# Optimization experiments

Measured on AMD Instinct MI355X. Metric: run time of the kernel, lower is better.

Reference implementation:

```python
import jax, jax.numpy as jnp
import numpy as np

NUM_HEADS = 4
EPS = 1e-5

def _proj(x, W, b):
    # 1x1x1 Conv3d == channel-wise linear: x [B,C,H,W,D], W [Cout,Cin], b [Cout]
    return jnp.einsum('oc,bchwd->bohwd', W, x) + b[None, :, None, None, None]

def setup_inputs() -> dict:
    key = jax.random.key(0)
    ks = jax.random.split(key, 12)
    B, C, H, W, D = 2, 128, 16, 16, 16
    s = 1.0 / np.sqrt(C)
    inp = {
        'query_features': jax.random.normal(ks[0], (B, C, H, W, D), jnp.float32),
        'key_value_features': jax.random.normal(ks[1], (B, C, H, W, D), jnp.float32),
        'Wq': jax.random.normal(ks[2], (C, C), jnp.float32) * s,
        'bq': jax.random.normal(ks[3], (C,), jnp.float32) * 0.01,
        'Wk': jax.random.normal(ks[4], (C, C), jnp.float32) * s,
        'bk': jax.random.normal(ks[5], (C,), jnp.float32) * 0.01,
        'Wv': jax.random.normal(ks[6], (C, C), jnp.float32) * s,
        'bv': jax.random.normal(ks[7], (C,), jnp.float32) * 0.01,
        'Wo': jax.random.normal(ks[8], (C, C), jnp.float32) * s,
        'bo': jax.random.normal(ks[9], (C,), jnp.float32) * 0.01,
    }
    return inp

def reference(query_features, key_value_features, Wq, bq, Wk, bk, Wv, bv, Wo, bo):
    B, C, H, W, D = query_features.shape
    hd = C // NUM_HEADS  # head_dim
    N = H * W * D
    Q = _proj(query_features, Wq, bq).reshape(B, NUM_HEADS, hd, N)
    K = _proj(key_value_features, Wk, bk).reshape(B, NUM_HEADS, hd, N)
    V = _proj(key_value_features, Wv, bv).reshape(B, NUM_HEADS, hd, N)
    scale = hd ** -0.5
    attn = jnp.einsum('bhdn,bhdm->bhnm', Q, K) * scale  # [B,h,N,N]
    attn = jax.nn.softmax(attn, axis=-1)
    out = jnp.einsum('bhnm,bhdm->bhdn', attn, V).reshape(B, C, H, W, D)
    out = _proj(out, Wo, bo)
    res = query_features + out
    # InstanceNorm3d (affine=False): normalize over spatial dims per (B,C)
    mu = jnp.mean(res, axis=(2, 3, 4), keepdims=True)
    var = jnp.var(res, axis=(2, 3, 4), keepdims=True)
    return (res - mu) * jax.lax.rsqrt(var + EPS)
```

## Files before the change

### kernel.cpp

```cpp
#include <hip/hip_runtime.h>
#include <hip/hip_bf16.h>

typedef unsigned short u16;
typedef unsigned int u32;
typedef __bf16 bf16_t;
typedef bf16_t bf16x8 __attribute__((ext_vector_type(8)));
typedef float f32x4 __attribute__((ext_vector_type(4)));

#define NTOT 4096
#define CCH 128
#define QSCL 0.25503486703f

__device__ __forceinline__ float bf2f(u16 x) {
    return __uint_as_float(((u32)x) << 16);
}
__device__ __forceinline__ u32 pkbf(float a, float b) {
    __hip_bfloat162 h = __float22bfloat162_rn(make_float2(a, b));
    u32 r; __builtin_memcpy(&r, &h, 4); return r;
}
__device__ __forceinline__ u16 f2bf(float a) {
    return (u16)(pkbf(a, a) & 0xffffu);
}

__global__ __launch_bounds__(256, 4) void proj_kernel(
    const float* __restrict__ xq, const float* __restrict__ xkv,
    const float* __restrict__ Wq, const float* __restrict__ bq_,
    const float* __restrict__ Wk, const float* __restrict__ bk_,
    const float* __restrict__ Wv, const float* __restrict__ bv_,
    u16* __restrict__ Qt, u16* __restrict__ Kt, u16* __restrict__ Vn)
{
    const int nt = blockIdx.x, p = blockIdx.y, b = blockIdx.z;
    const float* X    = (p == 0) ? xq : xkv;
    const float* W    = (p == 0) ? Wq : (p == 1) ? Wk : Wv;
    const float* bias = (p == 0) ? bq_ : (p == 1) ? bk_ : bv_;
    const float scl   = (p == 0) ? QSCL : 1.0f;
    const int n0 = nt * 64;
    const int tid = threadIdx.x;

    __shared__ u16 Xt[64 * 128];
    __shared__ u16 Wl[128 * 136];

    #pragma unroll
    for (int k = 0; k < 4; ++k) {
        int n = tid & 63;
        int c = (tid >> 6) + k * 4;
        float f[8];
        #pragma unroll
        for (int j = 0; j < 8; ++j)
            f[j] = X[((size_t)(b * CCH) + 8 * c + j) * NTOT + n0 + n];
        uint4 vv = {pkbf(f[0], f[1]), pkbf(f[2], f[3]), pkbf(f[4], f[5]), pkbf(f[6], f[7])};
        *(uint4*)(Xt + n * 128 + ((c ^ (n & 7)) * 8)) = vv;
    }
    #pragma unroll
    for (int k = 0; k < 8; ++k) {
        int id = tid + k * 256;
        int row = id >> 4;
        int off = (id & 15) * 8;
        const float* wsrc = W + (size_t)row * 128 + off;
        float4 f0 = *(const float4*)(wsrc);
        float4 f1 = *(const float4*)(wsrc + 4);
        uint4 vv = {pkbf(f0.x * scl, f0.y * scl), pkbf(f0.z * scl, f0.w * scl),
                    pkbf(f1.x * scl, f1.y * scl), pkbf(f1.z * scl, f1.w * scl)};
        *(uint4*)(Wl + row * 136 + off) = vv;
    }
    __syncthreads();

    const int wave = tid >> 6, lane = tid & 63;
    const int quad = lane >> 4, l16 = lane & 15;
    f32x4 acc[8];
    #pragma unroll
    for (int cf = 0; cf < 8; ++cf) acc[cf] = (f32x4){0.f, 0.f, 0.f, 0.f};

    #pragma unroll
    for (int kk = 0; kk < 4; ++kk) {
        bf16x8 bx = *(const bf16x8*)(Xt + (wave * 16 + l16) * 128 +
                                     (((kk * 4 + quad) ^ (l16 & 7)) * 8));
        #pragma unroll
        for (int cf = 0; cf < 8; ++cf) {
            bf16x8 aw = *(const bf16x8*)(Wl + (cf * 16 + l16) * 136 + kk * 32 + quad * 8);
            acc[cf] = __builtin_amdgcn_mfma_f32_16x16x32_bf16(aw, bx, acc[cf], 0, 0, 0);
        }
    }

    const int n = n0 + wave * 16 + l16;
    #pragma unroll
    for (int cf = 0; cf < 8; ++cf) {
        float4 b4 = *(const float4*)(bias + cf * 16 + quad * 4);
        float v0 = acc[cf][0] + b4.x * scl;
        float v1 = acc[cf][1] + b4.y * scl;
        float v2 = acc[cf][2] + b4.z * scl;
        float v3 = acc[cf][3] + b4.w * scl;
        if (p < 2) {
            const int h = cf >> 1;
            const int d0 = (cf & 1) * 16 + quad * 4;
            u16* dst = (p == 0 ? Qt : Kt) + ((size_t)(b * 4 + h) * NTOT + n) * 32 + d0;
            uint2 vv = {pkbf(v0, v1), pkbf(v2, v3)};
            *(uint2*)dst = vv;
        } else {
            int c = cf * 16 + quad * 4;
            u16* dst = Vn + (size_t)(b * CCH + c) * NTOT + n;
            dst[0 * NTOT] = f2bf(v0); dst[1 * NTOT] = f2bf(v1);
            dst[2 * NTOT] = f2bf(v2); dst[3 * NTOT] = f2bf(v3);
        }
    }
}

__global__ __launch_bounds__(256, 2) void flash_attn_kernel(
    const u16* __restrict__ Qt, const u16* __restrict__ Kt,
    const u16* __restrict__ Vn, u16* __restrict__ pO, float* __restrict__ pL)
{
    const int bh = blockIdx.z, kc = blockIdx.y;
    const int wave = threadIdx.x >> 6, lane = threadIdx.x & 63;
    const int q = lane >> 4, l16 = lane & 15;
    const int q0w = blockIdx.x * 256 + wave * 64;

    const u16* Qbh = Qt + (size_t)bh * NTOT * 32;
    const u16* Kbh = Kt + (size_t)bh * NTOT * 32;
    const u16* Vg  = Vn + ((size_t)((bh >> 2) * CCH + (bh & 3) * 32)) * NTOT;

    __shared__ u16 Kb[2][2048];
    __shared__ u16 Vb[2][2048];
    __shared__ u16 Pb[4][1024];

    const int kbase = kc * 512;

    bf16x8 bq[4];
    #pragma unroll
    for (int g = 0; g < 4; ++g)
        bq[g] = *(const bf16x8*)(Qbh + (size_t)(q0w + g * 16 + l16) * 32 + q * 8);

    const size_t ksrc = (size_t)(wave * 16 + l16) * 32 + q * 8;
    const size_t vsrc = (size_t)((wave & 1) * 16 + l16) * NTOT + (wave >> 1) * 32 + q * 8;
    const int kv_dst = wave * 512 + lane * 8;

    uint4 kreg = *(const uint4*)(Kbh + (size_t)kbase * 32 + ksrc);
    uint4 vreg = *(const uint4*)(Vg + vsrc + kbase);
    *(uint4*)(&Kb[0][kv_dst]) = kreg;
    *(uint4*)(&Vb[0][kv_dst]) = vreg;
    __syncthreads();

    f32x4 o[4][2];
    #pragma unroll
    for (int g = 0; g < 4; ++g) {
        o[g][0] = (f32x4){0,0,0,0};
        o[g][1] = (f32x4){0,0,0,0};
    }
    const f32x4 zero = {0,0,0,0};
    float lp[4] = {0.f, 0.f, 0.f, 0.f};

    u16* pw = &Pb[wave][0];
    const int pwr = (q >> 1) * 128 + l16 * 8 + (q & 1) * 4;
    const int prd0 = 0 * 512 + lane * 8;
    const int prd1 = 1 * 512 + lane * 8;

    for (int it = 0; it < 8; ++it) {
        const int cur = it & 1;
        if (it < 7) {
            const int m1 = kbase + (it + 1) * 64;
            kreg = *(const uint4*)(Kbh + (size_t)m1 * 32 + ksrc);
            vreg = *(const uint4*)(Vg + vsrc + m1);
        }
        f32x4 s[4][4];
        #pragma unroll
        for (int t = 0; t < 4; ++t) {
            bf16x8 ak = *(const bf16x8*)(&Kb[cur][t * 512 + lane * 8]);
            #pragma unroll
            for (int g = 0; g < 4; ++g)
                s[g][t] = __builtin_amdgcn_mfma_f32_16x16x32_bf16(ak, bq[g], zero, 0, 0, 0);
        }
        bf16x8 av00 = *(const bf16x8*)(&Vb[cur][0 * 512 + lane * 8]);
        bf16x8 av01 = *(const bf16x8*)(&Vb[cur][1 * 512 + lane * 8]);
        bf16x8 av10 = *(const bf16x8*)(&Vb[cur][2 * 512 + lane * 8]);
        bf16x8 av11 = *(const bf16x8*)(&Vb[cur][3 * 512 + lane * 8]);
        #pragma unroll
        for (int g = 0; g < 4; ++g) {
            #pragma unroll
            for (int t = 0; t < 4; ++t) {
                float p0 = __builtin_amdgcn_exp2f(s[g][t][0]);
                float p1 = __builtin_amdgcn_exp2f(s[g][t][1]);
                float p2 = __builtin_amdgcn_exp2f(s[g][t][2]);
                float p3 = __builtin_amdgcn_exp2f(s[g][t][3]);
                lp[g] += (p0 + p1) + (p2 + p3);
                uint2 wv = {pkbf(p0, p1), pkbf(p2, p3)};
                *(uint2*)(pw + (t >> 1) * 512 + (t & 1) * 256 + pwr) = wv;
            }
            bf16x8 pb0 = *(const bf16x8*)(pw + prd0);
            bf16x8 pb1 = *(const bf16x8*)(pw + prd1);
            o[g][0] = __builtin_amdgcn_mfma_f32_16x16x32_bf16(av00, pb0, o[g][0], 0, 0, 0);
            o[g][1] = __builtin_amdgcn_mfma_f32_16x16x32_bf16(av01, pb0, o[g][1], 0, 0, 0);
            o[g][0] = __builtin_amdgcn_mfma_f32_16x16x32_bf16(av10, pb1, o[g][0], 0, 0, 0);
            o[g][1] = __builtin_amdgcn_mfma_f32_16x16x32_bf16(av11, pb1, o[g][1], 0, 0, 0);
        }
        if (it < 7) {
            const int nb = (it + 1) & 1;
            *(uint4*)(&Kb[nb][kv_dst]) = kreg;
            *(uint4*)(&Vb[nb][kv_dst]) = vreg;
        }
        __syncthreads();
    }

    #pragma unroll
    for (int g = 0; g < 4; ++g) {
        lp[g] += __shfl_xor(lp[g], 16);
        lp[g] += __shfl_xor(lp[g], 32);
        const size_t ob = ((size_t)(kc * 8 + bh) * NTOT + q0w + g * 16 + l16) * 32 + q * 4;
        uint2 w0 = {pkbf(o[g][0][0], o[g][0][1]), pkbf(o[g][0][2], o[g][0][3])};
        uint2 w1 = {pkbf(o[g][1][0], o[g][1][1]), pkbf(o[g][1][2], o[g][1][3])};
        *(uint2*)(pO + ob)      = w0;
        *(uint2*)(pO + ob + 16) = w1;
        if (q == 0)
            pL[(size_t)(kc * 8 + bh) * NTOT + q0w + g * 16 + l16] = lp[g];
    }
}

__global__ __launch_bounds__(256, 4) void outproj_kernel(
    const float* __restrict__ xq,
    const u16* __restrict__ pO, const float* __restrict__ pL,
    const float* __restrict__ Wo, const float* __restrict__ bo,
    float* __restrict__ res, float* __restrict__ partS, float* __restrict__ partQ)
{
    const int nt = blockIdx.x, ct = blockIdx.y, b = blockIdx.z;
    const int n0 = nt * 64;
    const int tid = threadIdx.x;

    __shared__ u16 Xt[64 * 128];
    __shared__ u16 Wl[64 * 136];

    #pragma unroll
    for (int k = 0; k < 4; ++k) {
        int cid = tid + k * 256;
        int n = cid >> 4;
        int ch = cid & 15;
        int bh = b * 4 + (ch >> 2);
        int d0 = (ch & 3) * 8;
        float l = 0.f;
        float v[8];
        #pragma unroll
        for (int j = 0; j < 8; ++j) v[j] = 0.f;
        #pragma unroll
        for (int kcc = 0; kcc < 8; ++kcc) {
            const size_t nrow = (size_t)(kcc * 8 + bh) * NTOT + n0 + n;
            l += pL[nrow];
            uint4 u = *(const uint4*)(pO + nrow * 32 + d0);
            const u32 uu[4] = {u.x, u.y, u.z, u.w};
            #pragma unroll
            for (int j = 0; j < 4; ++j) {
                v[2 * j]     += bf2f((u16)(uu[j] & 0xffffu));
                v[2 * j + 1] += bf2f((u16)(uu[j] >> 16));
            }
        }
        const float inv = 1.0f / l;
        uint4 vv = {pkbf(v[0] * inv, v[1] * inv), pkbf(v[2] * inv, v[3] * inv),
                    pkbf(v[4] * inv, v[5] * inv), pkbf(v[6] * inv, v[7] * inv)};
        *(uint4*)(Xt + n * 128 + ((ch ^ (n & 7)) * 8)) = vv;
    }
    #pragma unroll
    for (int k = 0; k < 4; ++k) {
        int id = tid + k * 256;
        int row = id >> 4;
        int off = (id & 15) * 8;
        const float* wsrc = Wo + (size_t)(ct * 64 + row) * 128 + off;
        float4 f0 = *(const float4*)(wsrc);
        float4 f1 = *(const float4*)(wsrc + 4);
        uint4 vv = {pkbf(f0.x, f0.y), pkbf(f0.z, f0.w),
                    pkbf(f1.x, f1.y), pkbf(f1.z, f1.w)};
        *(uint4*)(Wl + row * 136 + off) = vv;
    }
    __syncthreads();

    const int wave = tid >> 6, lane = tid & 63;
    const int quad = lane >> 4, l16 = lane & 15;
    f32x4 acc[4];
    #pragma unroll
    for (int cf = 0; cf < 4; ++cf) acc[cf] = (f32x4){0.f, 0.f, 0.f, 0.f};

    #pragma unroll
    for (int kk = 0; kk < 4; ++kk) {
        bf16x8 bx = *(const bf16x8*)(Xt + (wave * 16 + l16) * 128 +
                                     (((kk * 4 + quad) ^ (l16 & 7)) * 8));
        #pragma unroll
        for (int cf = 0; cf < 4; ++cf) {
            bf16x8 aw = *(const bf16x8*)(Wl + (cf * 16 + l16) * 136 + kk * 32 + quad * 8);
            acc[cf] = __builtin_amdgcn_mfma_f32_16x16x32_bf16(aw, bx, acc[cf], 0, 0, 0);
        }
    }

    const int n = n0 + wave * 16 + l16;
    const int tile = nt * 4 + wave;
    #pragma unroll
    for (int cf = 0; cf < 4; ++cf) {
        float4 b4 = *(const float4*)(bo + ct * 64 + cf * 16 + quad * 4);
        const float bb[4] = {b4.x, b4.y, b4.z, b4.w};
        float sv[4], qv[4];
        #pragma unroll
        for (int r = 0; r < 4; ++r) {
            int c = ct * 64 + cf * 16 + quad * 4 + r;
            float v = acc[cf][r] + bb[r] + xq[(size_t)(b * CCH + c) * NTOT + n];
            res[(size_t)(b * CCH + c) * NTOT + n] = v;
            sv[r] = v;
            qv[r] = v * v;
        }
        #pragma unroll
        for (int off = 1; off < 16; off <<= 1) {
            #pragma unroll
            for (int r = 0; r < 4; ++r) {
                sv[r] += __shfl_xor(sv[r], off);
                qv[r] += __shfl_xor(qv[r], off);
            }
        }
        if (l16 == 0) {
            #pragma unroll
            for (int r = 0; r < 4; ++r) {
                int c = ct * 64 + cf * 16 + quad * 4 + r;
                partS[(size_t)(b * CCH + c) * 256 + tile] = sv[r];
                partQ[(size_t)(b * CCH + c) * 256 + tile] = qv[r];
            }
        }
    }
}

__global__ __launch_bounds__(256) void norm_kernel(
    const float* __restrict__ res, const float* __restrict__ partS,
    const float* __restrict__ partQ, float* __restrict__ out)
{
    const int c = blockIdx.x, b = blockIdx.y;
    const int tid = threadIdx.x;
    const size_t row = (size_t)(b * CCH + c);
    __shared__ float rs[4], rq[4];
    float s = partS[row * 256 + tid];
    float q = partQ[row * 256 + tid];
    #pragma unroll
    for (int off = 1; off < 64; off <<= 1) {
        s += __shfl_xor(s, off);
        q += __shfl_xor(q, off);
    }
    const int wv = tid >> 6, ln = tid & 63;
    if (ln == 0) { rs[wv] = s; rq[wv] = q; }
    __syncthreads();
    float ts = rs[0] + rs[1] + rs[2] + rs[3];
    float tq = rq[0] + rq[1] + rq[2] + rq[3];
    float mu  = ts * (1.0f / 4096.0f);
    float var = tq * (1.0f / 4096.0f) - mu * mu;
    float inv = rsqrtf(var + 1e-5f);
    const size_t base = row * NTOT;
    #pragma unroll
    for (int j = 0; j < 4; ++j) {
        int n = tid * 4 + j * 1024;
        float4 v = *(const float4*)(res + base + n);
        float4 o;
        o.x = (v.x - mu) * inv; o.y = (v.y - mu) * inv;
        o.z = (v.z - mu) * inv; o.w = (v.w - mu) * inv;
        *(float4*)(out + base + n) = o;
    }
}

extern "C" void kernel_launch(void* const* d_in, const int* in_sizes, int n_in,
                              void* d_out, int out_size, void* d_ws, size_t ws_size,
                              hipStream_t stream)
{
    const float* xq  = (const float*)d_in[0];
    const float* xkv = (const float*)d_in[1];
    const float* Wq  = (const float*)d_in[2];
    const float* bq  = (const float*)d_in[3];
    const float* Wk  = (const float*)d_in[4];
    const float* bk  = (const float*)d_in[5];
    const float* Wv  = (const float*)d_in[6];
    const float* bv  = (const float*)d_in[7];
    const float* Wo  = (const float*)d_in[8];
    const float* bo  = (const float*)d_in[9];
    float* out = (float*)d_out;

    char* ws = (char*)d_ws;
    const size_t MB = (size_t)1 << 20;
    u16* Qt = (u16*)(ws + 0 * MB);
    u16* Kt = (u16*)(ws + 2 * MB);
    u16* Vn = (u16*)(ws + 4 * MB);
    u16* pO = (u16*)(ws + 6 * MB);
    float* pL = (float*)(ws + 22 * MB);
    float* res   = (float*)(ws + 23 * MB);
    float* partS = (float*)(ws + 27 * MB);
    float* partQ = (float*)(ws + 27 * MB + 262144);

    proj_kernel<<<dim3(64, 3, 2), 256, 0, stream>>>(xq, xkv, Wq, bq, Wk, bk, Wv, bv, Qt, Kt, Vn);
    flash_attn_kernel<<<dim3(16, 8, 8), 256, 0, stream>>>(Qt, Kt, Vn, pO, pL);
    outproj_kernel<<<dim3(64, 2, 2), 256, 0, stream>>>(xq, pO, pL, Wo, bo, res, partS, partQ);
    norm_kernel<<<dim3(128, 2), 256, 0, stream>>>(res, partS, partQ, out);
}
```

Baseline: 127.2 us.

## Split attention KV range finer and reduce partials with float atomics

The KV dimension is split into 16 chunks instead of 8, which doubles the attention grid to 2048 blocks with half the loop iterations each. Each block now atomically adds its fp32 partial outputs and row sums into a shared accumulator, replacing the bf16 per-chunk partial buffers. proj_kernel zeroes that accumulator, and outproj reads a single normalized row instead of summing 8 partials. This trades partial-buffer traffic and reduction work for many global float atomics, whose summation order is nondeterministic.

```diff
diff --git a/kernel.cpp b/kernel.cpp
--- a/kernel.cpp
+++ b/kernel.cpp
@@ -10,6 +10,7 @@
 #define NTOT 4096
 #define CCH 128
 #define QSCL 0.25503486703f
+#define NZERO_F4 278528
 
 __device__ __forceinline__ float bf2f(u16 x) {
     return __uint_as_float(((u32)x) << 16);
@@ -27,15 +28,28 @@
     const float* __restrict__ Wq, const float* __restrict__ bq_,
     const float* __restrict__ Wk, const float* __restrict__ bk_,
     const float* __restrict__ Wv, const float* __restrict__ bv_,
-    u16* __restrict__ Qt, u16* __restrict__ Kt, u16* __restrict__ Vn)
+    u16* __restrict__ Qt, u16* __restrict__ Kt, u16* __restrict__ Vn,
+    float* __restrict__ attnAcc)
 {
     const int nt = blockIdx.x, p = blockIdx.y, b = blockIdx.z;
+    const int tid = threadIdx.x;
+
+    {
+        const int bid = nt + 64 * (p + 3 * b);
+        float4* zp = (float4*)attnAcc;
+        const float4 z4 = {0.f, 0.f, 0.f, 0.f};
+        #pragma unroll
+        for (int z = 0; z < 3; ++z) {
+            int idx = bid * 768 + z * 256 + tid;
+            if (idx < NZERO_F4) zp[idx] = z4;
+        }
+    }
+
     const float* X    = (p == 0) ? xq : xkv;
     const float* W    = (p == 0) ? Wq : (p == 1) ? Wk : Wv;
     const float* bias = (p == 0) ? bq_ : (p == 1) ? bk_ : bv_;
     const float scl   = (p == 0) ? QSCL : 1.0f;
     const int n0 = nt * 64;
-    const int tid = threadIdx.x;
 
     __shared__ u16 Xt[64 * 128];
     __shared__ u16 Wl[128 * 136];
@@ -107,7 +121,8 @@
 
 __global__ __launch_bounds__(256, 2) void flash_attn_kernel(
     const u16* __restrict__ Qt, const u16* __restrict__ Kt,
-    const u16* __restrict__ Vn, u16* __restrict__ pO, float* __restrict__ pL)
+    const u16* __restrict__ Vn, float* __restrict__ attnAcc,
+    float* __restrict__ pLsum)
 {
     const int bh = blockIdx.z, kc = blockIdx.y;
     const int wave = threadIdx.x >> 6, lane = threadIdx.x & 63;
@@ -122,7 +137,7 @@
     __shared__ u16 Vb[2][2048];
     __shared__ u16 Pb[4][1024];
 
-    const int kbase = kc * 512;
+    const int kbase = kc * 256;
 
     bf16x8 bq[4];
     #pragma unroll
@@ -153,9 +168,9 @@
     const int prd0 = 0 * 512 + lane * 8;
     const int prd1 = 1 * 512 + lane * 8;
 
-    for (int it = 0; it < 8; ++it) {
+    for (int it = 0; it < 4; ++it) {
         const int cur = it & 1;
-        if (it < 7) {
+        if (it < 3) {
             const int m1 = kbase + (it + 1) * 64;
             kreg = *(const uint4*)(Kbh + (size_t)m1 * 32 + ksrc);
             vreg = *(const uint4*)(Vg + vsrc + m1);
@@ -191,7 +206,7 @@
             o[g][0] = __builtin_amdgcn_mfma_f32_16x16x32_bf16(av10, pb1, o[g][0], 0, 0, 0);
             o[g][1] = __builtin_amdgcn_mfma_f32_16x16x32_bf16(av11, pb1, o[g][1], 0, 0, 0);
         }
-        if (it < 7) {
+        if (it < 3) {
             const int nb = (it + 1) & 1;
             *(uint4*)(&Kb[nb][kv_dst]) = kreg;
             *(uint4*)(&Vb[nb][kv_dst]) = vreg;
@@ -199,23 +214,25 @@
         __syncthreads();
     }
 
+    float* abase = attnAcc + ((size_t)bh * NTOT + q0w + l16) * 32 + q * 4;
     #pragma unroll
     for (int g = 0; g < 4; ++g) {
         lp[g] += __shfl_xor(lp[g], 16);
         lp[g] += __shfl_xor(lp[g], 32);
-        const size_t ob = ((size_t)(kc * 8 + bh) * NTOT + q0w + g * 16 + l16) * 32 + q * 4;
-        uint2 w0 = {pkbf(o[g][0][0], o[g][0][1]), pkbf(o[g][0][2], o[g][0][3])};
-        uint2 w1 = {pkbf(o[g][1][0], o[g][1][1]), pkbf(o[g][1][2], o[g][1][3])};
-        *(uint2*)(pO + ob)      = w0;
-        *(uint2*)(pO + ob + 16) = w1;
+        float* ag = abase + (size_t)g * 16 * 32;
+        #pragma unroll
+        for (int r = 0; r < 4; ++r) {
+            atomicAdd(ag + r,      o[g][0][r]);
+            atomicAdd(ag + 16 + r, o[g][1][r]);
+        }
         if (q == 0)
-            pL[(size_t)(kc * 8 + bh) * NTOT + q0w + g * 16 + l16] = lp[g];
+            atomicAdd(&pLsum[(size_t)bh * NTOT + q0w + g * 16 + l16], lp[g]);
     }
 }
 
 __global__ __launch_bounds__(256, 4) void outproj_kernel(
     const float* __restrict__ xq,
-    const u16* __restrict__ pO, const float* __restrict__ pL,
+    const float* __restrict__ attnAcc, const float* __restrict__ pLsum,
     const float* __restrict__ Wo, const float* __restrict__ bo,
     float* __restrict__ res, float* __restrict__ partS, float* __restrict__ partQ)
 {
@@ -233,25 +250,12 @@
         int ch = cid & 15;
         int bh = b * 4 + (ch >> 2);
         int d0 = (ch & 3) * 8;
-        float l = 0.f;
-        float v[8];
-        #pragma unroll
-        for (int j = 0; j < 8; ++j) v[j] = 0.f;
-        #pragma unroll
-        for (int kcc = 0; kcc < 8; ++kcc) {
-            const size_t nrow = (size_t)(kcc * 8 + bh) * NTOT + n0 + n;
-            l += pL[nrow];
-            uint4 u = *(const uint4*)(pO + nrow * 32 + d0);
-            const u32 uu[4] = {u.x, u.y, u.z, u.w};
-            #pragma unroll
-            for (int j = 0; j < 4; ++j) {
-                v[2 * j]     += bf2f((u16)(uu[j] & 0xffffu));
-                v[2 * j + 1] += bf2f((u16)(uu[j] >> 16));
-            }
-        }
-        const float inv = 1.0f / l;
-        uint4 vv = {pkbf(v[0] * inv, v[1] * inv), pkbf(v[2] * inv, v[3] * inv),
-                    pkbf(v[4] * inv, v[5] * inv), pkbf(v[6] * inv, v[7] * inv)};
+        const float* src = attnAcc + ((size_t)bh * NTOT + n0 + n) * 32 + d0;
+        float inv = 1.0f / pLsum[(size_t)bh * NTOT + n0 + n];
+        float4 f0 = *(const float4*)(src);
+        float4 f1 = *(const float4*)(src + 4);
+        uint4 vv = {pkbf(f0.x * inv, f0.y * inv), pkbf(f0.z * inv, f0.w * inv),
+                    pkbf(f1.x * inv, f1.y * inv), pkbf(f1.z * inv, f1.w * inv)};
         *(uint4*)(Xt + n * 128 + ((ch ^ (n & 7)) * 8)) = vv;
     }
     #pragma unroll
@@ -375,14 +379,14 @@
     u16* Qt = (u16*)(ws + 0 * MB);
     u16* Kt = (u16*)(ws + 2 * MB);
     u16* Vn = (u16*)(ws + 4 * MB);
-    u16* pO = (u16*)(ws + 6 * MB);
-    float* pL = (float*)(ws + 22 * MB);
-    float* res   = (float*)(ws + 23 * MB);
+    float* attnAcc = (float*)(ws + 6 * MB);
+    float* pLsum   = (float*)(ws + 10 * MB);
+    float* res   = (float*)(ws + 11 * MB);
     float* partS = (float*)(ws + 27 * MB);
     float* partQ = (float*)(ws + 27 * MB + 262144);
 
-    proj_kernel<<<dim3(64, 3, 2), 256, 0, stream>>>(xq, xkv, Wq, bq, Wk, bk, Wv, bv, Qt, Kt, Vn);
-    flash_attn_kernel<<<dim3(16, 8, 8), 256, 0, stream>>>(Qt, Kt, Vn, pO, pL);
-    outproj_kernel<<<dim3(64, 2, 2), 256, 0, stream>>>(xq, pO, pL, Wo, bo, res, partS, partQ);
+    proj_kernel<<<dim3(64, 3, 2), 256, 0, stream>>>(xq, xkv, Wq, bq, Wk, bk, Wv, bv, Qt, Kt, Vn, attnAcc);
+    flash_attn_kernel<<<dim3(16, 16, 8), 256, 0, stream>>>(Qt, Kt, Vn, attnAcc, pLsum);
+    outproj_kernel<<<dim3(64, 2, 2), 256, 0, stream>>>(xq, attnAcc, pLsum, Wo, bo, res, partS, partQ);
     norm_kernel<<<dim3(128, 2), 256, 0, stream>>>(res, partS, partQ, out);
 }
```

After: 371.8 us. +192.2%, slower.
